# Performance work log

Hardware: AMD Instinct MI355X
Metric: run time of the kernel (lower is better)

## Reference

```python
import jax, jax.numpy as jnp
import numpy as np

EPS = 1e-12

def _l2norm(x):
    return x * jax.lax.rsqrt(jnp.maximum(jnp.sum(x * x, -1, keepdims=True), EPS))

def _reverse_seq(x, lens):
    # per-row reversal of the first `lens[b]` steps (tf.reverse_sequence semantics)
    T = x.shape[1]
    ar = jnp.arange(T)[None, :]
    idx = jnp.where(ar < lens[:, None], lens[:, None] - 1 - ar, ar)
    return jnp.take_along_axis(x, idx[:, :, None], axis=1)

def _lstm(x, lens, Wx, Wh, b):
    # x: [B,T,D]; outputs zeroed past lens, state frozen past lens (dynamic_rnn)
    B, T, _ = x.shape
    H = Wh.shape[0]
    xW = jnp.einsum('btd,dh->bth', x, Wx) + b  # [B,T,4H]
    def step(carry, inp):
        h, c = carry
        xw_t, t = inp
        gates = xw_t + h @ Wh
        i, f, g, o = jnp.split(gates, 4, axis=-1)
        c_new = jax.nn.sigmoid(f) * c + jax.nn.sigmoid(i) * jnp.tanh(g)
        h_new = jax.nn.sigmoid(o) * jnp.tanh(c_new)
        valid = (t < lens)[:, None]
        return (jnp.where(valid, h_new, h), jnp.where(valid, c_new, c)), jnp.where(valid, h_new, 0.0)
    z = jnp.zeros((B, H), x.dtype)
    _, outs = jax.lax.scan(step, (z, z), (xW.transpose(1, 0, 2), jnp.arange(T)))
    return outs.transpose(1, 0, 2)

def _bilstm(x, lens, Wx_f, Wh_f, b_f, Wx_b, Wh_b, b_b):
    fwd = _lstm(x, lens, Wx_f, Wh_f, b_f)
    bwd = _reverse_seq(_lstm(_reverse_seq(x, lens), lens, Wx_b, Wh_b, b_b), lens)
    return jnp.concatenate([fwd, bwd], -1)  # [B,T,2R]

def setup_inputs() -> dict:
    B, T, CTX, D, R, HA, TD = 4096, 80, 10, 300, 200, 100, 256
    V, NTOK, NTY, PL = 100000, 250, 113, 3
    ks = jax.random.split(jax.random.key(0), 16)
    f32 = jnp.float32
    return {
        'input_data': jax.random.randint(ks[0], (B, T), 0, V, jnp.int32),
        'entMentIndex': jax.random.randint(ks[1], (B, 5), 0, B * T, jnp.int32),
        'entCtxLeftIndex': jax.random.randint(ks[2], (B, CTX), 0, B * T, jnp.int32),
        'entCtxRightIndex': jax.random.randint(ks[3], (B, CTX), 0, B * T, jnp.int32),
        'entMentLent': jnp.full((B, 1), 5.0, f32),
        'ctxLeftLent': jnp.full((B, 1), float(CTX), f32),
        'ctxRightLent': jnp.full((B, 1), float(CTX), f32),
        'type_path': jax.random.randint(ks[4], (NTY, PL), 0, NTOK, jnp.int32),
        'word_embed': jax.random.normal(ks[5], (V, D), f32) * 0.1,
        'h_m': jax.random.normal(ks[6], (D, HA), f32) * 0.01,
        'h1': jax.random.normal(ks[7], (2 * R, HA), f32) * 0.01,
        'h2': jax.random.normal(ks[8], (HA, 1), f32) * 0.01,
        'Wx_f': jax.random.normal(ks[9], (D, 4 * R), f32) * 0.05,
        'Wh_f': jax.random.normal(ks[10], (R, 4 * R), f32) * 0.05,
        'b_f': jnp.zeros((4 * R,), f32),
        'Wx_b': jax.random.normal(ks[11], (D, 4 * R), f32) * 0.05,
        'Wh_b': jax.random.normal(ks[12], (R, 4 * R), f32) * 0.05,
        'b_b': jnp.zeros((4 * R,), f32),
        'dense_W': jax.random.normal(ks[13], (D + 2 * R, TD), f32) * 0.05,
        'dense_b': jnp.zeros((TD,), f32),
        'type_tok': jax.random.normal(ks[14], (NTOK, TD), f32) * 0.01,
    }

def reference(input_data, entMentIndex, entCtxLeftIndex, entCtxRightIndex,
              entMentLent, ctxLeftLent, ctxRightLent, type_path, word_embed,
              h_m, h1, h2, Wx_f, Wh_f, b_f, Wx_b, Wh_b, b_b,
              dense_W, dense_b, type_tok):
    D = word_embed.shape[1]
    # flattened sentence embeddings with zero padding row at the end
    flat = jnp.concatenate(
        [jnp.take(word_embed, input_data.reshape(-1), axis=0),
         jnp.zeros((1, D), word_embed.dtype)], 0)
    # mention feature: mean of mention word vectors
    f1 = jnp.take(flat, entMentIndex, axis=0).sum(1) / entMentLent  # [B,D]
    # context features via shared BiLSTM
    left = jnp.take(flat, entCtxLeftIndex, axis=0)
    right = jnp.take(flat, entCtxRightIndex, axis=0)
    f2 = _bilstm(left, ctxLeftLent[:, 0].astype(jnp.int32), Wx_f, Wh_f, b_f, Wx_b, Wh_b, b_b)
    f3 = _bilstm(right, ctxRightLent[:, 0].astype(jnp.int32), Wx_f, Wh_f, b_f, Wx_b, Wh_b, b_b)
    ctx = jnp.concatenate([f2, f3], 1)  # [B, 2*CTX, 2R]
    # attention pooling (non-BBN branch uses relu)
    att = jax.nn.relu(jnp.einsum('btr,rh->bth', ctx, h1) + (f1 @ h_m)[:, None, :])
    w = jax.nn.softmax((att @ h2)[:, :, 0], axis=-1)  # [B, 2*CTX]
    ctx_feat = jnp.einsum('btr,bt->br', ctx, w)
    feat = jnp.concatenate([f1, ctx_feat], 1)  # [B, D+2R]
    ent = _l2norm(jax.nn.relu(feat @ dense_W + dense_b))  # [B, TD]
    # type-path embeddings: sum token embeddings along path, l2-normalize
    type_pad = jnp.concatenate([type_tok, jnp.zeros((1, type_tok.shape[1]), type_tok.dtype)], 0)
    type_norm = _l2norm(jnp.take(type_pad, type_path, axis=0).sum(1))  # [NTY, TD]
    return ent @ type_norm.T  # [B, NTY]
```

## Files before the change

### kernel.cpp

```cpp
#include <hip/hip_runtime.h>
#include <hip/hip_bf16.h>

constexpr int B    = 4096;
constexpr int T    = 80;
constexpr int CTXN = 10;
constexpr int D    = 300;
constexpr int R    = 200;
constexpr int HA   = 100;
constexpr int TD   = 256;
constexpr int NTY  = 113;
constexpr int PL   = 3;
constexpr int NTOK = 250;
constexpr int CTX2 = 20;
constexpr int R2   = 400;
constexpr int FEAT = 700;

constexpr int XSB  = 320;
constexpr int KH   = 256;
constexpr int KW   = 576;
constexpr int NB   = 832;
constexpr int CTXS = 448;
constexpr int F1S  = 320;
constexpr int FBS  = 704;
constexpr int FMS  = 128;
constexpr int MX   = 2 * B * CTXN;

typedef __attribute__((ext_vector_type(8))) short bf16x8;
typedef __attribute__((ext_vector_type(4))) float f32x4;

__device__ __forceinline__ ushort f2bf(float f) {
    union { float f; uint32_t u; } x{f};
    uint32_t r = x.u + 0x7fff + ((x.u >> 16) & 1);
    return (ushort)(r >> 16);
}
__device__ __forceinline__ float bf2f(ushort u) {
    union { uint32_t u; float f; } x{(uint32_t)u << 16};
    return x.f;
}

#define GLD_LDS(g, l) __builtin_amdgcn_global_load_lds( \
    (const __attribute__((address_space(1))) void*)(g), \
    (__attribute__((address_space(3))) void*)(l), 16, 0, 0)

constexpr int NWC = 2 * NB * KW;
__global__ void k_prepw3(const float* __restrict__ Wx_f, const float* __restrict__ Wh_f,
                         const float* __restrict__ bf_, const float* __restrict__ Wx_b,
                         const float* __restrict__ Wh_b, const float* __restrict__ bb_,
                         ushort* __restrict__ Wcat, float* __restrict__ biasb) {
    int gid = blockIdx.x * blockDim.x + threadIdx.x;
    if (gid < NWC) {
        int k = gid % KW;
        int q = gid / KW;
        int np = q % NB, dir = q / NB;
        int rb = np >> 6, g = (np >> 4) & 3, ri = np & 15;
        int r = rb * 16 + ri, col = g * 200 + r;
        float v = 0.f;
        if (r < R) {
            if (k < KH) {
                if (k < R) v = (dir ? Wh_b : Wh_f)[(size_t)k * 800 + col];
            } else {
                int kx = k - KH;
                if (kx < D) v = (dir ? Wx_b : Wx_f)[(size_t)kx * 800 + col];
            }
        }
        Wcat[gid] = f2bf(v);
    } else if (gid < NWC + 2 * NB) {
        int t = gid - NWC;
        int np = t % NB, dirb = t / NB;
        int rb = np >> 6, g = (np >> 4) & 3, ri = np & 15;
        int r = rb * 16 + ri, col = g * 200 + r;
        biasb[t] = (r < R) ? (dirb ? bb_ : bf_)[col] : 0.f;
    }
}

__global__ void k_preph1(const float* __restrict__ h1, ushort* __restrict__ h1t) {
    int gid = blockIdx.x * blockDim.x + threadIdx.x;
    if (gid >= FMS * CTXS) return;
    int k = gid % CTXS, n = gid / CTXS;
    float v = (n < HA && k < R2) ? h1[(size_t)k * HA + n] : 0.f;
    h1t[gid] = f2bf(v);
}
__global__ void k_prephm(const float* __restrict__ h_m, ushort* __restrict__ h_mt) {
    int gid = blockIdx.x * blockDim.x + threadIdx.x;
    if (gid >= FMS * F1S) return;
    int k = gid % F1S, n = gid / F1S;
    float v = (n < HA && k < D) ? h_m[(size_t)k * HA + n] : 0.f;
    h_mt[gid] = f2bf(v);
}
__global__ void k_prepdw(const float* __restrict__ dW, ushort* __restrict__ dWt) {
    int gid = blockIdx.x * blockDim.x + threadIdx.x;
    if (gid >= TD * FBS) return;
    int k = gid % FBS, n = gid / FBS;
    float v = (k < FEAT) ? dW[(size_t)k * TD + n] : 0.f;
    dWt[gid] = f2bf(v);
}

__global__ void k_gatherb(const int* __restrict__ idxL, const int* __restrict__ idxR,
                          const int* __restrict__ input_data,
                          const float* __restrict__ we,
                          ushort* __restrict__ xb) {
    int row = blockIdx.x * 4 + (threadIdx.x >> 6);
    int lane = threadIdx.x & 63;
    if (row >= MX) return;
    int side = row / (B * CTXN);
    int bt = row % (B * CTXN);
    int idx = (side ? idxR : idxL)[bt];
    int w = (idx >= 0 && idx < B * T) ? input_data[idx] : -1;
    ushort* dst = xb + (size_t)row * XSB;
    if (lane < XSB / 8) {
        int e0 = lane * 8;
        ushort tmp[8];
        #pragma unroll
        for (int j = 0; j < 8; ++j) {
            int e = e0 + j;
            float f = (w >= 0 && e < D) ? we[(size_t)w * D + e] : 0.f;
            tmp[j] = f2bf(f);
        }
        *reinterpret_cast<bf16x8*>(dst + e0) = *reinterpret_cast<bf16x8*>(tmp);
    }
}

__global__ void k_f1(const int* __restrict__ ment_idx,
                     const float* __restrict__ ment_lent,
                     const int* __restrict__ input_data,
                     const float* __restrict__ we,
                     ushort* __restrict__ featb, ushort* __restrict__ f1b) {
    int b = blockIdx.x;
    __shared__ int wrow[5];
    if (threadIdx.x < 5) {
        int idx = ment_idx[b * 5 + threadIdx.x];
        wrow[threadIdx.x] = (idx >= 0 && idx < B * T) ? input_data[idx] : -1;
    }
    __syncthreads();
    float inv = 1.0f / ment_lent[b];
    for (int d = threadIdx.x; d < F1S; d += blockDim.x) {
        float s = 0.f;
        if (d < D) {
            #pragma unroll
            for (int j = 0; j < 5; ++j) {
                int w = wrow[j];
                if (w >= 0) s += we[(size_t)w * D + d];
            }
            s *= inv;
        }
        ushort u = f2bf(s);
        if (d < D) featb[(size_t)b * FBS + d] = u;
        f1b[(size_t)b * F1S + d] = u;
    }
}

template<int MODE>
__global__ __launch_bounds__(256) void k_mfma(
    const ushort* __restrict__ A, int lda,
    const ushort* __restrict__ Bt, int ldb,
    float* __restrict__ C, int ldc, int K,
    const float* __restrict__ aux) {
    __shared__ __align__(16) ushort As[128 * 64];
    __shared__ __align__(16) ushort Bs[64 * 64];
    int tid = threadIdx.x, wave = tid >> 6, lane = tid & 63;
    int m0 = blockIdx.y * 128, n0 = blockIdx.x * 64;
    int wr = wave >> 1, wc = wave & 1;
    f32x4 acc[4][2] = {};

    for (int k0 = 0; k0 < K; k0 += 64) {
        #pragma unroll
        for (int p = 0; p < 4; ++p) {
            int chunk = p * 4 + wave;
            int row = chunk * 8 + (lane >> 3);
            int ss = (lane & 7) ^ (row & 7);
            GLD_LDS(A + (size_t)(m0 + row) * lda + k0 + ss * 8, As + chunk * 512);
        }
        #pragma unroll
        for (int p = 0; p < 2; ++p) {
            int chunk = p * 4 + wave;
            int row = chunk * 8 + (lane >> 3);
            int ss = (lane & 7) ^ (row & 7);
            GLD_LDS(Bt + (size_t)(n0 + row) * ldb + k0 + ss * 8, Bs + chunk * 512);
        }
        __syncthreads();
        #pragma unroll
        for (int kk = 0; kk < 2; ++kk) {
            bf16x8 a[4], bf[2];
            #pragma unroll
            for (int m = 0; m < 4; ++m) {
                int r = wr * 64 + m * 16 + (lane & 15);
                int ss = (kk * 4 + (lane >> 4)) ^ (r & 7);
                a[m] = *(const bf16x8*)&As[r * 64 + ss * 8];
            }
            #pragma unroll
            for (int n = 0; n < 2; ++n) {
                int r = wc * 32 + n * 16 + (lane & 15);
                int ss = (kk * 4 + (lane >> 4)) ^ (r & 7);
                bf[n] = *(const bf16x8*)&Bs[r * 64 + ss * 8];
            }
            #pragma unroll
            for (int m = 0; m < 4; ++m)
                #pragma unroll
                for (int n = 0; n < 2; ++n)
                    acc[m][n] = __builtin_amdgcn_mfma_f32_16x16x32_bf16(a[m], bf[n], acc[m][n], 0, 0, 0);
        }
        __syncthreads();
    }
    #pragma unroll
    for (int m = 0; m < 4; ++m) {
        #pragma unroll
        for (int n = 0; n < 2; ++n) {
            int c = n0 + wc * 32 + n * 16 + (lane & 15);
            #pragma unroll
            for (int j = 0; j < 4; ++j) {
                int rr = m0 + wr * 64 + m * 16 + (lane >> 4) * 4 + j;
                float v = acc[m][n][j];
                if (MODE == 1) v = fmaxf(v + aux[c], 0.f);
                C[(size_t)rr * ldc + c] = v;
            }
        }
    }
}

__global__ __launch_bounds__(512, 1) void k_lstm(
    const ushort* __restrict__ xb,
    const ushort* __restrict__ Wcat,
    const float* __restrict__ biasb,
    const float* __restrict__ lentL, const float* __restrict__ lentR,
    ushort* __restrict__ ctxb) {
    __shared__ __align__(16) ushort hS[64 * 256];
    __shared__ __align__(16) ushort xS[64 * 320];
    __shared__ __align__(16) ushort wS[8][2][2048];
    __shared__ int lenS[64];
    __shared__ int xrowS[CTXN][64];

    const int tid = threadIdx.x, wave = tid >> 6, lane = tid & 63;
    const int z = blockIdx.x >> 6, rg = blockIdx.x & 63;
    const int side = z >> 1, dir = z & 1;
    const int b0 = rg * 64;
    const ushort* Wd = Wcat + (size_t)dir * NB * KW;
    const int rl = lane & 15, ch = lane >> 4;

    if (tid < 64) {
        int b = b0 + tid;
        int len = (int)((side ? lentR : lentL)[b]);
        len = min(max(len, 0), CTXN);
        lenS[tid] = len;
        for (int s = 0; s < CTXN; ++s) {
            int tt = dir ? ((s < len) ? (len - 1 - s) : s) : s;
            xrowS[s][tid] = (side * (B * CTXN) + b * CTXN + tt) * XSB;
        }
    }
    {
        uint4 zz{0, 0, 0, 0};
        for (int i = tid; i < 64 * 256 / 8; i += 512)
            reinterpret_cast<uint4*>(hS)[i] = zz;
    }

    const int nrb = (wave + 8 < 13) ? 2 : 1;
    float bias_[2][4];
    #pragma unroll
    for (int g = 0; g < 4; ++g) {
        bias_[0][g] = biasb[dir * NB + wave * 64 + g * 16 + rl];
        bias_[1][g] = (nrb > 1) ? biasb[dir * NB + (wave + 8) * 64 + g * 16 + rl] : 0.f;
    }
    float cst[2][16];
    #pragma unroll
    for (int i = 0; i < 2; ++i)
        #pragma unroll
        for (int j = 0; j < 16; ++j) cst[i][j] = 0.f;

    __syncthreads();

    #pragma unroll
    for (int i = 0; i < 5; ++i) {
        int chunk = wave * 5 + i;
        int p = chunk * 64 + lane;
        int row = p / 40, c8s = p - row * 40;
        int c8 = c8s ^ (row & 7);
        GLD_LDS(xb + xrowS[0][row] + c8 * 8, xS + chunk * 512);
    }
    __syncthreads();

    float hnew[2][16];

    for (int s = 0; s < CTXN; ++s) {
        const int kstart = (s == 0) ? KH : 0;
        #pragma unroll
        for (int rbi = 0; rbi < 2; ++rbi) {
            if (rbi < nrb) {
                const int rb = rbi ? (wave + 8) : wave;
                const ushort* wb = Wd + (size_t)rb * 64 * KW;
                const int nit = (KW - kstart) >> 5;
                f32x4 acc[4][4];
                #pragma unroll
                for (int m = 0; m < 4; ++m)
                    #pragma unroll
                    for (int g = 0; g < 4; ++g) acc[m][g] = f32x4{0.f, 0.f, 0.f, 0.f};

                #pragma unroll
                for (int i = 0; i < 4; ++i) {
                    int p = i * 64 + lane;
                    int n = p >> 2, c8s = p & 3;
                    int c8 = c8s ^ ((n >> 1) & 3);
                    GLD_LDS(wb + (size_t)n * KW + kstart + c8 * 8, &wS[wave][0][0] + i * 512);
                }
                for (int t = 0; t < nit; ++t) {
                    int k0 = kstart + t * 32;
                    if (t + 1 < nit) {
                        int k1 = k0 + 32;
                        ushort* dst = &wS[wave][(t + 1) & 1][0];
                        #pragma unroll
                        for (int i = 0; i < 4; ++i) {
                            int p = i * 64 + lane;
                            int n = p >> 2, c8s = p & 3;
                            int c8 = c8s ^ ((n >> 1) & 3);
                            GLD_LDS(wb + (size_t)n * KW + k1 + c8 * 8, dst + i * 512);
                        }
                        asm volatile("s_waitcnt vmcnt(4)" ::: "memory");
                    } else {
                        asm volatile("s_waitcnt vmcnt(0)" ::: "memory");
                    }
                    const ushort* abase; int astr, kof;
                    if (k0 < KH) { abase = hS; astr = 256; kof = k0 >> 3; }
                    else         { abase = xS; astr = 320; kof = (k0 - KH) >> 3; }
                    bf16x8 af[4];
                    #pragma unroll
                    for (int m = 0; m < 4; ++m) {
                        int row = m * 16 + rl;
                        int g = (kof + ch) ^ (row & 7);
                        af[m] = *reinterpret_cast<const bf16x8*>(&abase[row * astr + g * 8]);
                    }
                    const ushort* wbuf = &wS[wave][t & 1][0];
                    bf16x8 bfr[4];
                    #pragma unroll
                    for (int g4 = 0; g4 < 4; ++g4) {
                        int col = g4 * 16 + rl;
                        int c8 = ch ^ ((rl >> 1) & 3);
                        bfr[g4] = *reinterpret_cast<const bf16x8*>(&wbuf[col * 32 + c8 * 8]);
                    }
                    #pragma unroll
                    for (int m = 0; m < 4; ++m)
                        #pragma unroll
                        for (int g4 = 0; g4 < 4; ++g4)
                            acc[m][g4] = __builtin_amdgcn_mfma_f32_16x16x32_bf16(
                                af[m], bfr[g4], acc[m][g4], 0, 0, 0);
                }
                #pragma unroll
                for (int m = 0; m < 4; ++m) {
                    #pragma unroll
                    for (int j = 0; j < 4; ++j) {
                        int row = m * 16 + ch * 4 + j;
                        float gi = acc[m][0][j] + bias_[rbi][0];
                        float gf = acc[m][1][j] + bias_[rbi][1];
                        float gg = acc[m][2][j] + bias_[rbi][2];
                        float go = acc[m][3][j] + bias_[rbi][3];
                        float si = 1.f / (1.f + __expf(-gi));
                        float sf = 1.f / (1.f + __expf(-gf));
                        float so = 1.f / (1.f + __expf(-go));
                        float cn = sf * cst[rbi][m * 4 + j] + si * tanhf(gg);
                        float hn = so * tanhf(cn);
                        if (s < lenS[row]) cst[rbi][m * 4 + j] = cn;
                        hnew[rbi][m * 4 + j] = hn;
                    }
                }
            }
        }
        asm volatile("s_waitcnt lgkmcnt(0)" ::: "memory");
        __builtin_amdgcn_s_barrier();

        #pragma unroll
        for (int rbi = 0; rbi < 2; ++rbi) {
            if (rbi < nrb) {
                const int rb = wave + rbi * 8;
                const int r = rb * 16 + rl;
                #pragma unroll
                for (int m = 0; m < 4; ++m) {
                    #pragma unroll
                    for (int j = 0; j < 4; ++j) {
                        int row = m * 16 + ch * 4 + j;
                        bool live = (s < lenS[row]);
                        ushort hv = f2bf(live ? hnew[rbi][m * 4 + j] : 0.f);
                        wS[wave][1][row * 32 + rbi * 16 + rl] = hv;
                        if (live && r < R)
                            hS[row * 256 + (((r >> 3) ^ (row & 7)) << 3) + (r & 7)] = hv;
                    }
                }
            }
        }
        if (s + 1 < CTXN) {
            #pragma unroll
            for (int i = 0; i < 5; ++i) {
                int chunk = wave * 5 + i;
                int p = chunk * 64 + lane;
                int row = p / 40, c8s = p - row * 40;
                int c8 = c8s ^ (row & 7);
                GLD_LDS(xb + xrowS[s + 1][row] + c8 * 8, xS + chunk * 512);
            }
        }
        asm volatile("s_waitcnt lgkmcnt(0)" ::: "memory");
        __builtin_amdgcn_s_barrier();

        for (int i = tid; i < 64 * 25; i += 512) {
            int row = i / 25, g = i - row * 25;
            int len = lenS[row];
            int tp = (s < len) ? (dir ? (len - 1 - s) : s) : s;
            int rb2 = g >> 1;
            int w = rb2 & 7, rbi = rb2 >> 3;
            int off = (g & 1) * 8;
            bf16x8 v = *reinterpret_cast<const bf16x8*>(&wS[w][1][row * 32 + rbi * 16 + off]);
            *reinterpret_cast<bf16x8*>(
                ctxb + ((size_t)(b0 + row) * CTX2 + side * CTXN + tp) * CTXS + dir * R + g * 8) = v;
        }
        asm volatile("s_waitcnt vmcnt(0) lgkmcnt(0)" ::: "memory");
        __builtin_amdgcn_s_barrier();
    }
}

__global__ __launch_bounds__(256) void k_attsc(
    const ushort* __restrict__ ctxb, const ushort* __restrict__ h1t,
    const float* __restrict__ fm, const float* __restrict__ h2,
    float* __restrict__ scores) {
    __shared__ __align__(16) ushort As[128 * 64];
    __shared__ __align__(16) ushort Bs[128 * 64];
    __shared__ float sred[128][2];
    __shared__ float h2s[128];
    int tid = threadIdx.x, wave = tid >> 6, lane = tid & 63;
    int m0 = blockIdx.x * 128;
    if (tid < 128) h2s[tid] = (tid < HA) ? h2[tid] : 0.f;
    int wr = wave >> 1, wc = wave & 1;
    f32x4 acc[4][4] = {};

    for (int k0 = 0; k0 < CTXS; k0 += 64) {
        #pragma unroll
        for (int p = 0; p < 4; ++p) {
            int chunk = p * 4 + wave;
            int row = chunk * 8 + (lane >> 3);
            int ss = (lane & 7) ^ (row & 7);
            GLD_LDS(ctxb + (size_t)(m0 + row) * CTXS + k0 + ss * 8, As + chunk * 512);
        }
        #pragma unroll
        for (int p = 0; p < 4; ++p) {
            int chunk = p * 4 + wave;
            int row = chunk * 8 + (lane >> 3);
            int ss = (lane & 7) ^ (row & 7);
            GLD_LDS(h1t + (size_t)row * CTXS + k0 + ss * 8, Bs + chunk * 512);
        }
        __syncthreads();
        #pragma unroll
        for (int kk = 0; kk < 2; ++kk) {
            bf16x8 a[4], bf[4];
            #pragma unroll
            for (int m = 0; m < 4; ++m) {
                int r = wr * 64 + m * 16 + (lane & 15);
                int ss = (kk * 4 + (lane >> 4)) ^ (r & 7);
                a[m] = *(const bf16x8*)&As[r * 64 + ss * 8];
            }
            #pragma unroll
            for (int n = 0; n < 4; ++n) {
                int r = wc * 64 + n * 16 + (lane & 15);
                int ss = (kk * 4 + (lane >> 4)) ^ (r & 7);
                bf[n] = *(const bf16x8*)&Bs[r * 64 + ss * 8];
            }
            #pragma unroll
            for (int m = 0; m < 4; ++m)
                #pragma unroll
                for (int n = 0; n < 4; ++n)
                    acc[m][n] = __builtin_amdgcn_mfma_f32_16x16x32_bf16(a[m], bf[n], acc[m][n], 0, 0, 0);
        }
        __syncthreads();
    }
    #pragma unroll
    for (int m = 0; m < 4; ++m) {
        #pragma unroll
        for (int j = 0; j < 4; ++j) {
            int rl = wr * 64 + m * 16 + (lane >> 4) * 4 + j;
            int brow = (m0 + rl) / CTX2;
            float v = 0.f;
            #pragma unroll
            for (int n = 0; n < 4; ++n) {
                int c = wc * 64 + n * 16 + (lane & 15);
                float a = acc[m][n][j] + fm[(size_t)brow * FMS + c];
                v += fmaxf(a, 0.f) * h2s[c];
            }
            #pragma unroll
            for (int o = 1; o < 16; o <<= 1) v += __shfl_xor(v, o, 64);
            if ((lane & 15) == 0) sred[rl][wc] = v;
        }
    }
    __syncthreads();
    if (tid < 128) scores[m0 + tid] = sred[tid][0] + sred[tid][1];
}

__global__ void k_att2(const float* __restrict__ scores,
                       const ushort* __restrict__ ctxb,
                       ushort* __restrict__ featb) {
    int b = blockIdx.x;
    float sc[CTX2];
    #pragma unroll
    for (int t = 0; t < CTX2; ++t) sc[t] = scores[b * CTX2 + t];
    float mx = -1e30f;
    #pragma unroll
    for (int t = 0; t < CTX2; ++t) mx = fmaxf(mx, sc[t]);
    float w[CTX2], sum = 0.f;
    #pragma unroll
    for (int t = 0; t < CTX2; ++t) { w[t] = __expf(sc[t] - mx); sum += w[t]; }
    float inv = 1.f / sum;
    for (int col = threadIdx.x; col < R2; col += 256) {
        float acc = 0.f;
        #pragma unroll
        for (int t = 0; t < CTX2; ++t)
            acc += w[t] * bf2f(ctxb[((size_t)b * CTX2 + t) * CTXS + col]);
        featb[(size_t)b * FBS + D + col] = f2bf(acc * inv);
    }
    if (threadIdx.x < FBS - FEAT)
        featb[(size_t)b * FBS + FEAT + threadIdx.x] = 0;
}

__device__ __forceinline__ float blk_sum_256(float v, float* red) {
    #pragma unroll
    for (int o = 32; o > 0; o >>= 1) v += __shfl_down(v, o, 64);
    int lane = threadIdx.x & 63, wid = threadIdx.x >> 6;
    if (lane == 0) red[wid] = v;
    __syncthreads();
    float t = red[0] + red[1] + red[2] + red[3];
    __syncthreads();
    return t;
}

__global__ void k_l2norm(float* __restrict__ x, int ncol) {
    int row = blockIdx.x;
    float* p = x + (size_t)row * ncol;
    __shared__ float red[4];
    float ss = 0.f;
    for (int c = threadIdx.x; c < ncol; c += 256) { float v = p[c]; ss += v * v; }
    float tot = blk_sum_256(ss, red);
    float scale = 1.f / sqrtf(fmaxf(tot, 1e-12f));
    for (int c = threadIdx.x; c < ncol; c += 256) p[c] *= scale;
}

__global__ void k_typenorm(const int* __restrict__ type_path,
                           const float* __restrict__ type_tok,
                           float* __restrict__ tnorm) {
    int y = blockIdx.x;
    int c = threadIdx.x;
    __shared__ float red[4];
    float s = 0.f;
    #pragma unroll
    for (int j = 0; j < PL; ++j) {
        int tk = type_path[y * PL + j];
        if (tk >= 0 && tk < NTOK) s += type_tok[(size_t)tk * TD + c];
    }
    float tot = blk_sum_256(s * s, red);
    float scale = 1.f / sqrtf(fmaxf(tot, 1e-12f));
    tnorm[(size_t)y * TD + c] = s * scale;
}

__global__ void k_final(const float* __restrict__ ent,
                        const float* __restrict__ tnorm,
                        float* __restrict__ out) {
    int b = blockIdx.x;
    __shared__ float es[TD];
    for (int c = threadIdx.x; c < TD; c += blockDim.x) es[c] = ent[(size_t)b * TD + c];
    __syncthreads();
    for (int y = threadIdx.x; y < NTY; y += blockDim.x) {
        const float* tn = tnorm + (size_t)y * TD;
        float acc = 0.f;
        #pragma unroll 4
        for (int k = 0; k < TD; ++k) acc += es[k] * tn[k];
        out[(size_t)b * NTY + y] = acc;
    }
}

static inline char* wsalloc(char*& p, size_t bytes) {
    char* r = p;
    p += (bytes + 255) & ~(size_t)255;
    return r;
}

extern "C" void kernel_launch(void* const* d_in, const int* in_sizes, int n_in,
                              void* d_out, int out_size, void* d_ws, size_t ws_size,
                              hipStream_t stream) {
    const int*   input_data       = (const int*)d_in[0];
    const int*   entMentIndex     = (const int*)d_in[1];
    const int*   entCtxLeftIndex  = (const int*)d_in[2];
    const int*   entCtxRightIndex = (const int*)d_in[3];
    const float* entMentLent      = (const float*)d_in[4];
    const float* ctxLeftLent      = (const float*)d_in[5];
    const float* ctxRightLent     = (const float*)d_in[6];
    const int*   type_path        = (const int*)d_in[7];
    const float* word_embed       = (const float*)d_in[8];
    const float* h_m              = (const float*)d_in[9];
    const float* h1               = (const float*)d_in[10];
    const float* h2               = (const float*)d_in[11];
    const float* Wx_f             = (const float*)d_in[12];
    const float* Wh_f             = (const float*)d_in[13];
    const float* b_f              = (const float*)d_in[14];
    const float* Wx_b             = (const float*)d_in[15];
    const float* Wh_b             = (const float*)d_in[16];
    const float* b_b              = (const float*)d_in[17];
    const float* dense_W          = (const float*)d_in[18];
    const float* dense_b          = (const float*)d_in[19];
    const float* type_tok         = (const float*)d_in[20];
    float* out = (float*)d_out;

    char* p = (char*)d_ws;
    ushort* xb    = (ushort*)wsalloc(p, (size_t)MX * XSB * 2);
    ushort* ctxb  = (ushort*)wsalloc(p, (size_t)B * CTX2 * CTXS * 2);
    ushort* featb = (ushort*)wsalloc(p, (size_t)B * FBS * 2);
    ushort* f1b   = (ushort*)wsalloc(p, (size_t)B * F1S * 2);
    float*  fm    = (float*) wsalloc(p, (size_t)B * FMS * 4);
    float*  scores= (float*) wsalloc(p, (size_t)MX * 4);
    float*  ent   = (float*) wsalloc(p, (size_t)B * TD * 4);
    float*  tnorm = (float*) wsalloc(p, (size_t)NTY * TD * 4);
    ushort* Wcat  = (ushort*)wsalloc(p, (size_t)2 * NB * KW * 2);
    float*  biasb = (float*) wsalloc(p, (size_t)2 * NB * 4);
    ushort* h1t   = (ushort*)wsalloc(p, (size_t)FMS * CTXS * 2);
    ushort* h_mt  = (ushort*)wsalloc(p, (size_t)FMS * F1S * 2);
    ushort* dWt   = (ushort*)wsalloc(p, (size_t)TD * FBS * 2);

    {
        int tot = NWC + 2 * NB;
        k_prepw3<<<(tot + 255) / 256, 256, 0, stream>>>(Wx_f, Wh_f, b_f, Wx_b, Wh_b, b_b,
                                                        Wcat, biasb);
    }
    k_preph1<<<(FMS * CTXS + 255) / 256, 256, 0, stream>>>(h1, h1t);
    k_prephm<<<(FMS * F1S + 255) / 256, 256, 0, stream>>>(h_m, h_mt);
    k_prepdw<<<(TD * FBS + 255) / 256, 256, 0, stream>>>(dense_W, dWt);

    k_gatherb<<<(MX + 3) / 4, 256, 0, stream>>>(entCtxLeftIndex, entCtxRightIndex,
                                                input_data, word_embed, xb);
    k_f1<<<B, 256, 0, stream>>>(entMentIndex, entMentLent, input_data, word_embed, featb, f1b);

    k_mfma<3><<<dim3(FMS / 64, B / 128), 256, 0, stream>>>(f1b, F1S, h_mt, F1S, fm, FMS, F1S, nullptr);

    k_lstm<<<256, 512, 0, stream>>>(xb, Wcat, biasb, ctxLeftLent, ctxRightLent, ctxb);

    k_attsc<<<MX / 128, 256, 0, stream>>>(ctxb, h1t, fm, h2, scores);
    k_att2<<<B, 256, 0, stream>>>(scores, ctxb, featb);

    k_mfma<1><<<dim3(TD / 64, B / 128), 256, 0, stream>>>(featb, FBS, dWt, FBS,
                                                          ent, TD, FBS, dense_b);
    k_l2norm<<<B, 256, 0, stream>>>(ent, TD);
    k_typenorm<<<NTY, TD, 0, stream>>>(type_path, type_tok, tnorm);
    k_final<<<B, 128, 0, stream>>>(ent, tnorm, out);
}
```

Measured before the change: 594.6 us.

## Load LSTM weights directly into registers from MFMA-tiled layout, prefetch x via registers

Pre-tiles the LSTM weights into per-(row-block, k-tile) 32x64 MFMA fragment layout so each wave loads B fragments straight from global into registers with double buffering, dropping the LDS staging buffer and its waitcnt loop. The next step's x rows are prefetched into registers during the GEMM and written to LDS afterward. Blocks are remapped so each XCD handles a single direction, which should improve L2 reuse of that direction's weights. It also uses fast rcp-based sigmoid/tanh, stages h in a dedicated LDS buffer, and removes one barrier per step. In exchange there is more register pressure and slightly lower activation precision.

```diff
diff --git a/kernel.cpp b/kernel.cpp
--- a/kernel.cpp
+++ b/kernel.cpp
@@ -19,6 +19,8 @@
 constexpr int KH   = 256;
 constexpr int KW   = 576;
 constexpr int NB   = 832;
+constexpr int NKT  = 18;
+constexpr int NRB  = 13;
 constexpr int CTXS = 448;
 constexpr int F1S  = 320;
 constexpr int FBS  = 704;
@@ -37,35 +39,43 @@
     union { uint32_t u; float f; } x{(uint32_t)u << 16};
     return x.f;
 }
+__device__ __forceinline__ float fsig(float x) {
+    return __builtin_amdgcn_rcpf(1.f + __expf(-x));
+}
+__device__ __forceinline__ float ftanh(float x) {
+    return 1.f - 2.f * __builtin_amdgcn_rcpf(__expf(2.f * x) + 1.f);
+}
 
 #define GLD_LDS(g, l) __builtin_amdgcn_global_load_lds( \
     (const __attribute__((address_space(1))) void*)(g), \
     (__attribute__((address_space(3))) void*)(l), 16, 0, 0)
 
-constexpr int NWC = 2 * NB * KW;
-__global__ void k_prepw3(const float* __restrict__ Wx_f, const float* __restrict__ Wh_f,
+constexpr int NW2 = 2 * NRB * NKT * 2048;
+__global__ void k_prepw4(const float* __restrict__ Wx_f, const float* __restrict__ Wh_f,
                          const float* __restrict__ bf_, const float* __restrict__ Wx_b,
                          const float* __restrict__ Wh_b, const float* __restrict__ bb_,
-                         ushort* __restrict__ Wcat, float* __restrict__ biasb) {
+                         ushort* __restrict__ W2, float* __restrict__ biasb) {
     int gid = blockIdx.x * blockDim.x + threadIdx.x;
-    if (gid < NWC) {
-        int k = gid % KW;
-        int q = gid / KW;
-        int np = q % NB, dir = q / NB;
-        int rb = np >> 6, g = (np >> 4) & 3, ri = np & 15;
-        int r = rb * 16 + ri, col = g * 200 + r;
+    if (gid < NW2) {
+        int e = gid & 2047, tile = gid >> 11;
+        int kt = tile % NKT, q = tile / NKT;
+        int rb = q % NRB, dir = q / NRB;
+        int col = e >> 5, kk = e & 31;
+        int k = kt * 32 + kk;
+        int g = col >> 4, ri = col & 15;
+        int r = rb * 16 + ri, ocol = g * 200 + r;
         float v = 0.f;
         if (r < R) {
             if (k < KH) {
-                if (k < R) v = (dir ? Wh_b : Wh_f)[(size_t)k * 800 + col];
+                if (k < R) v = (dir ? Wh_b : Wh_f)[(size_t)k * 800 + ocol];
             } else {
                 int kx = k - KH;
-                if (kx < D) v = (dir ? Wx_b : Wx_f)[(size_t)kx * 800 + col];
-            }
-        }
-        Wcat[gid] = f2bf(v);
-    } else if (gid < NWC + 2 * NB) {
-        int t = gid - NWC;
+                if (kx < D) v = (dir ? Wx_b : Wx_f)[(size_t)kx * 800 + ocol];
+            }
+        }
+        W2[gid] = f2bf(v);
+    } else if (gid < NW2 + 2 * NB) {
+        int t = gid - NW2;
         int np = t % NB, dirb = t / NB;
         int rb = np >> 6, g = (np >> 4) & 3, ri = np & 15;
         int r = rb * 16 + ri, col = g * 200 + r;
@@ -217,23 +227,57 @@
     }
 }
 
+#define LOADW(dst, tp) { _Pragma("unroll") for (int g4 = 0; g4 < 4; ++g4) \
+    dst[g4] = *reinterpret_cast<const bf16x8*>((tp) + (g4 * 16 + rl) * 32 + ch * 8); }
+
+#define AREAD(kt, af) { \
+    const ushort* abase = ((kt) < 8) ? hS : xS; \
+    const int astr = ((kt) < 8) ? 256 : 320; \
+    const int kof = ((kt) < 8) ? (kt) * 4 : ((kt) - 8) * 4; \
+    _Pragma("unroll") for (int m = 0; m < 4; ++m) { \
+        int row = m * 16 + rl; \
+        int g = (kof + ch) ^ (row & 7); \
+        af[m] = *reinterpret_cast<const bf16x8*>(&abase[row * astr + g * 8]); } }
+
+#define MFMA16(af, Bv) { _Pragma("unroll") for (int m = 0; m < 4; ++m) \
+    _Pragma("unroll") for (int g4 = 0; g4 < 4; ++g4) \
+        acc[m][g4] = __builtin_amdgcn_mfma_f32_16x16x32_bf16(af[m], Bv[g4], acc[m][g4], 0, 0, 0); }
+
+#define RB_GEMM(KT0, NIT) { \
+    const ushort* wt = Wd2 + ((size_t)rb * NKT + (KT0)) * 2048; \
+    bf16x8 BA[4], BB[4]; \
+    LOADW(BA, wt); LOADW(BB, wt + 2048); \
+    _Pragma("unroll") \
+    for (int t = 0; t < (NIT); t += 2) { \
+        bf16x8 af[4]; \
+        AREAD((KT0) + t, af); MFMA16(af, BA); \
+        if (t + 2 < (NIT)) LOADW(BA, wt + (t + 2) * 2048); \
+        AREAD((KT0) + t + 1, af); MFMA16(af, BB); \
+        if (t + 3 < (NIT)) LOADW(BB, wt + (t + 3) * 2048); \
+    } }
+
+#define BARRIER_LGKM() { asm volatile("s_waitcnt lgkmcnt(0)" ::: "memory"); \
+    __builtin_amdgcn_s_barrier(); }
+
 __global__ __launch_bounds__(512, 1) void k_lstm(
     const ushort* __restrict__ xb,
-    const ushort* __restrict__ Wcat,
+    const ushort* __restrict__ W2,
     const float* __restrict__ biasb,
     const float* __restrict__ lentL, const float* __restrict__ lentR,
     ushort* __restrict__ ctxb) {
     __shared__ __align__(16) ushort hS[64 * 256];
     __shared__ __align__(16) ushort xS[64 * 320];
-    __shared__ __align__(16) ushort wS[8][2][2048];
+    __shared__ __align__(16) ushort hst[2][64][208];
     __shared__ int lenS[64];
     __shared__ int xrowS[CTXN][64];
 
     const int tid = threadIdx.x, wave = tid >> 6, lane = tid & 63;
-    const int z = blockIdx.x >> 6, rg = blockIdx.x & 63;
-    const int side = z >> 1, dir = z & 1;
+    const int bid = blockIdx.x, xcd = bid & 7;
+    const int dir = xcd >> 2;
+    const int idx = (xcd & 3) * 32 + (bid >> 3);
+    const int side = idx >> 6, rg = idx & 63;
     const int b0 = rg * 64;
-    const ushort* Wd = Wcat + (size_t)dir * NB * KW;
+    const ushort* Wd2 = W2 + (size_t)dir * NRB * NKT * 2048;
     const int rl = lane & 15, ch = lane >> 4;
 
     if (tid < 64) {
@@ -251,8 +295,7 @@
         for (int i = tid; i < 64 * 256 / 8; i += 512)
             reinterpret_cast<uint4*>(hS)[i] = zz;
     }
-
-    const int nrb = (wave + 8 < 13) ? 2 : 1;
+    const int nrb = (wave + 8 < NRB) ? 2 : 1;
     float bias_[2][4];
     #pragma unroll
     for (int g = 0; g < 4; ++g) {
@@ -277,70 +320,24 @@
     }
     __syncthreads();
 
-    float hnew[2][16];
-
     for (int s = 0; s < CTXN; ++s) {
-        const int kstart = (s == 0) ? KH : 0;
+        const int cb = s & 1;
+        uint4 xreg[5];
+        if (s + 1 < CTXN) {
+            #pragma unroll
+            for (int i = 0; i < 5; ++i) {
+                int p = (wave * 5 + i) * 64 + lane;
+                int row = p / 40, c8s = p - row * 40;
+                int c8 = c8s ^ (row & 7);
+                xreg[i] = *reinterpret_cast<const uint4*>(xb + xrowS[s + 1][row] + c8 * 8);
+            }
+        }
         #pragma unroll
         for (int rbi = 0; rbi < 2; ++rbi) {
             if (rbi < nrb) {
-                const int rb = rbi ? (wave + 8) : wave;
-                const ushort* wb = Wd + (size_t)rb * 64 * KW;
-                const int nit = (KW - kstart) >> 5;
-                f32x4 acc[4][4];
-                #pragma unroll
-                for (int m = 0; m < 4; ++m)
-                    #pragma unroll
-                    for (int g = 0; g < 4; ++g) acc[m][g] = f32x4{0.f, 0.f, 0.f, 0.f};
-
-                #pragma unroll
-                for (int i = 0; i < 4; ++i) {
-                    int p = i * 64 + lane;
-                    int n = p >> 2, c8s = p & 3;
-                    int c8 = c8s ^ ((n >> 1) & 3);
-                    GLD_LDS(wb + (size_t)n * KW + kstart + c8 * 8, &wS[wave][0][0] + i * 512);
-                }
-                for (int t = 0; t < nit; ++t) {
-                    int k0 = kstart + t * 32;
-                    if (t + 1 < nit) {
-                        int k1 = k0 + 32;
-                        ushort* dst = &wS[wave][(t + 1) & 1][0];
-                        #pragma unroll
-                        for (int i = 0; i < 4; ++i) {
-                            int p = i * 64 + lane;
-                            int n = p >> 2, c8s = p & 3;
-                            int c8 = c8s ^ ((n >> 1) & 3);
-                            GLD_LDS(wb + (size_t)n * KW + k1 + c8 * 8, dst + i * 512);
-                        }
-                        asm volatile("s_waitcnt vmcnt(4)" ::: "memory");
-                    } else {
-                        asm volatile("s_waitcnt vmcnt(0)" ::: "memory");
-                    }
-                    const ushort* abase; int astr, kof;
-                    if (k0 < KH) { abase = hS; astr = 256; kof = k0 >> 3; }
-                    else         { abase = xS; astr = 320; kof = (k0 - KH) >> 3; }
-                    bf16x8 af[4];
-                    #pragma unroll
-                    for (int m = 0; m < 4; ++m) {
-                        int row = m * 16 + rl;
-                        int g = (kof + ch) ^ (row & 7);
-                        af[m] = *reinterpret_cast<const bf16x8*>(&abase[row * astr + g * 8]);
-                    }
-                    const ushort* wbuf = &wS[wave][t & 1][0];
-                    bf16x8 bfr[4];
-                    #pragma unroll
-                    for (int g4 = 0; g4 < 4; ++g4) {
-                        int col = g4 * 16 + rl;
-                        int c8 = ch ^ ((rl >> 1) & 3);
-                        bfr[g4] = *reinterpret_cast<const bf16x8*>(&wbuf[col * 32 + c8 * 8]);
-                    }
-                    #pragma unroll
-                    for (int m = 0; m < 4; ++m)
-                        #pragma unroll
-                        for (int g4 = 0; g4 < 4; ++g4)
-                            acc[m][g4] = __builtin_amdgcn_mfma_f32_16x16x32_bf16(
-                                af[m], bfr[g4], acc[m][g4], 0, 0, 0);
-                }
+                const int rb = wave + rbi * 8;
+                f32x4 acc[4][4] = {};
+                if (s == 0) { RB_GEMM(8, 10) } else { RB_GEMM(0, 18) }
                 #pragma unroll
                 for (int m = 0; m < 4; ++m) {
                     #pragma unroll
@@ -350,35 +347,35 @@
                         float gf = acc[m][1][j] + bias_[rbi][1];
                         float gg = acc[m][2][j] + bias_[rbi][2];
                         float go = acc[m][3][j] + bias_[rbi][3];
-                        float si = 1.f / (1.f + __expf(-gi));
-                        float sf = 1.f / (1.f + __expf(-gf));
-                        float so = 1.f / (1.f + __expf(-go));
-                        float cn = sf * cst[rbi][m * 4 + j] + si * tanhf(gg);
-                        float hn = so * tanhf(cn);
-                        if (s < lenS[row]) cst[rbi][m * 4 + j] = cn;
-                        hnew[rbi][m * 4 + j] = hn;
+                        float si = fsig(gi), sf = fsig(gf), so = fsig(go);
+                        float cn = sf * cst[rbi][m * 4 + j] + si * ftanh(gg);
+                        float hn = so * ftanh(cn);
+                        bool live = (s < lenS[row]);
+                        if (live) cst[rbi][m * 4 + j] = cn;
+                        int r = rb * 16 + rl;
+                        hst[cb][row][r] = f2bf((live && r < R) ? hn : 0.f);
                     }
                 }
             }
         }
-        asm volatile("s_waitcnt lgkmcnt(0)" ::: "memory");
-        __builtin_amdgcn_s_barrier();
+        BARRIER_LGKM();
 
         #pragma unroll
         for (int rbi = 0; rbi < 2; ++rbi) {
             if (rbi < nrb) {
                 const int rb = wave + rbi * 8;
                 const int r = rb * 16 + rl;
-                #pragma unroll
-                for (int m = 0; m < 4; ++m) {
+                if (r < R) {
                     #pragma unroll
-                    for (int j = 0; j < 4; ++j) {
-                        int row = m * 16 + ch * 4 + j;
-                        bool live = (s < lenS[row]);
-                        ushort hv = f2bf(live ? hnew[rbi][m * 4 + j] : 0.f);
-                        wS[wave][1][row * 32 + rbi * 16 + rl] = hv;
-                        if (live && r < R)
-                            hS[row * 256 + (((r >> 3) ^ (row & 7)) << 3) + (r & 7)] = hv;
+                    for (int m = 0; m < 4; ++m) {
+                        #pragma unroll
+                        for (int j = 0; j < 4; ++j) {
+                            int row = m * 16 + ch * 4 + j;
+                            if (s < lenS[row]) {
+                                ushort hv = hst[cb][row][r];
+                                hS[row * 256 + ((((r >> 3) ^ (row & 7)) << 3) | (r & 7))] = hv;
+                            }
+                        }
                     }
                 }
             }
@@ -386,29 +383,21 @@
         if (s + 1 < CTXN) {
             #pragma unroll
             for (int i = 0; i < 5; ++i) {
-                int chunk = wave * 5 + i;
-                int p = chunk * 64 + lane;
-                int row = p / 40, c8s = p - row * 40;
-                int c8 = c8s ^ (row & 7);
-                GLD_LDS(xb + xrowS[s + 1][row] + c8 * 8, xS + chunk * 512);
-            }
-        }
-        asm volatile("s_waitcnt lgkmcnt(0)" ::: "memory");
-        __builtin_amdgcn_s_barrier();
+                int p = (wave * 5 + i) * 64 + lane;
+                *reinterpret_cast<bf16x8*>(&xS[p * 8]) =
+                    *reinterpret_cast<const bf16x8*>(&xreg[i]);
+            }
+        }
+        BARRIER_LGKM();
 
         for (int i = tid; i < 64 * 25; i += 512) {
             int row = i / 25, g = i - row * 25;
             int len = lenS[row];
             int tp = (s < len) ? (dir ? (len - 1 - s) : s) : s;
-            int rb2 = g >> 1;
-            int w = rb2 & 7, rbi = rb2 >> 3;
-            int off = (g & 1) * 8;
-            bf16x8 v = *reinterpret_cast<const bf16x8*>(&wS[w][1][row * 32 + rbi * 16 + off]);
+            bf16x8 v = *reinterpret_cast<const bf16x8*>(&hst[cb][row][g * 8]);
             *reinterpret_cast<bf16x8*>(
                 ctxb + ((size_t)(b0 + row) * CTX2 + side * CTXN + tp) * CTXS + dir * R + g * 8) = v;
         }
-        asm volatile("s_waitcnt vmcnt(0) lgkmcnt(0)" ::: "memory");
-        __builtin_amdgcn_s_barrier();
     }
 }
 
@@ -608,16 +597,16 @@
     float*  scores= (float*) wsalloc(p, (size_t)MX * 4);
     float*  ent   = (float*) wsalloc(p, (size_t)B * TD * 4);
     float*  tnorm = (float*) wsalloc(p, (size_t)NTY * TD * 4);
-    ushort* Wcat  = (ushort*)wsalloc(p, (size_t)2 * NB * KW * 2);
+    ushort* W2    = (ushort*)wsalloc(p, (size_t)NW2 * 2);
     float*  biasb = (float*) wsalloc(p, (size_t)2 * NB * 4);
     ushort* h1t   = (ushort*)wsalloc(p, (size_t)FMS * CTXS * 2);
     ushort* h_mt  = (ushort*)wsalloc(p, (size_t)FMS * F1S * 2);
     ushort* dWt   = (ushort*)wsalloc(p, (size_t)TD * FBS * 2);
 
     {
-        int tot = NWC + 2 * NB;
-        k_prepw3<<<(tot + 255) / 256, 256, 0, stream>>>(Wx_f, Wh_f, b_f, Wx_b, Wh_b, b_b,
-                                                        Wcat, biasb);
+        int tot = NW2 + 2 * NB;
+        k_prepw4<<<(tot + 255) / 256, 256, 0, stream>>>(Wx_f, Wh_f, b_f, Wx_b, Wh_b, b_b,
+                                                        W2, biasb);
     }
     k_preph1<<<(FMS * CTXS + 255) / 256, 256, 0, stream>>>(h1, h1t);
     k_prephm<<<(FMS * F1S + 255) / 256, 256, 0, stream>>>(h_m, h_mt);
@@ -629,7 +618,7 @@
 
     k_mfma<3><<<dim3(FMS / 64, B / 128), 256, 0, stream>>>(f1b, F1S, h_mt, F1S, fm, FMS, F1S, nullptr);
 
-    k_lstm<<<256, 512, 0, stream>>>(xb, Wcat, biasb, ctxLeftLent, ctxRightLent, ctxb);
+    k_lstm<<<256, 512, 0, stream>>>(xb, W2, biasb, ctxLeftLent, ctxRightLent, ctxb);
 
     k_attsc<<<MX / 128, 256, 0, stream>>>(ctxb, h1t, fm, h2, scores);
     k_att2<<<B, 256, 0, stream>>>(scores, ctxb, featb);
```

Measured after the change: 907.0 us. 1.53x slower.
